# Kernel tuning notes

Hardware: AMD Instinct MI355X
Metric: run time of the kernel (lower is better)

The kernel has to match this reference:

```python
import jax, jax.numpy as jnp
import numpy as np

B = 128           # persons in batch
V = 128           # visits per person
CPV = 16          # codes per visit
MAX_VISITS = 510  # 512 - 2, hard-coded in module
D = 256           # embedding_dim * n_heads = 128 * 2
H = 2             # n_heads
DH = D // H
MAX_DAYS = 365
VOCAB = 30000
N_LAYERS = 2
DFF = 4 * D


def setup_inputs() -> dict:
    key = jax.random.key(0)
    ks = jax.random.split(key, 24)
    total_visits = B * V
    total_codes = total_visits * CPV
    all_codes = jax.random.randint(ks[0], (total_codes,), 0, VOCAB, dtype=jnp.int32)
    # code -> visit segment id (contiguous, as produced by the per-person loop)
    seg_ids = (jnp.arange(total_codes, dtype=jnp.int32) // CPV).astype(jnp.int32)
    # visit -> flattened slot in padded [B, MAX_VISITS] tensor (right-aligned)
    pos = MAX_VISITS - V + jnp.arange(V, dtype=jnp.int32)
    dest = (jnp.arange(B, dtype=jnp.int32)[:, None] * MAX_VISITS + pos[None, :]).reshape(-1)
    times = jax.random.uniform(ks[1], (total_visits,), minval=0.0, maxval=float(MAX_DAYS), dtype=jnp.float32)
    s = 0.02
    concept_emb = jax.random.normal(ks[2], (VOCAB, D), dtype=jnp.float32) * s
    pad_emb = jnp.zeros((D,), dtype=jnp.float32)
    Wq = jax.random.normal(ks[3], (N_LAYERS, D, D), dtype=jnp.float32) * s
    Wk = jax.random.normal(ks[4], (N_LAYERS, D, D), dtype=jnp.float32) * s
    Wv = jax.random.normal(ks[5], (N_LAYERS, D, D), dtype=jnp.float32) * s
    Wo = jax.random.normal(ks[6], (N_LAYERS, D, D), dtype=jnp.float32) * s
    W1 = jax.random.normal(ks[7], (N_LAYERS, D, DFF), dtype=jnp.float32) * s
    W2 = jax.random.normal(ks[8], (N_LAYERS, DFF, D), dtype=jnp.float32) * s
    z = lambda *sh: jnp.zeros(sh, dtype=jnp.float32)
    o = lambda *sh: jnp.ones(sh, dtype=jnp.float32)
    return dict(all_codes=all_codes, seg_ids=seg_ids, dest=dest, times=times,
                concept_emb=concept_emb, pad_emb=pad_emb,
                Wq=Wq, Wk=Wk, Wv=Wv, Wo=Wo,
                bq=z(N_LAYERS, D), bk=z(N_LAYERS, D), bv=z(N_LAYERS, D), bo=z(N_LAYERS, D),
                ln1_g=o(N_LAYERS, D), ln1_b=z(N_LAYERS, D),
                W1=W1, b1=z(N_LAYERS, DFF), W2=W2, b2=z(N_LAYERS, D),
                ln2_g=o(N_LAYERS, D), ln2_b=z(N_LAYERS, D))


def _ln(x, g, b):
    m = jnp.mean(x, axis=-1, keepdims=True)
    v = jnp.var(x, axis=-1, keepdims=True)
    return g * (x - m) * jax.lax.rsqrt(v + 1e-5) + b


def _forward(all_codes, seg_ids, dest, times, concept_emb, pad_emb,
             Wq, Wk, Wv, Wo, bq, bk, bv, bo, ln1_g, ln1_b,
             W1, b1, W2, b2, ln2_g, ln2_b):
    # gather code embeddings and segment-sum per visit (index_add_ in torch)
    emb = concept_emb[all_codes]                               # [total_codes, D]
    summed = jax.ops.segment_sum(emb, seg_ids, num_segments=B * V)  # [B*V, D]
    # scatter visits right-aligned into padded [B*MAX_VISITS, D], pad slots = pad_emb
    padded = jnp.broadcast_to(pad_emb, (B * MAX_VISITS, D)).at[dest].set(summed)
    # sinusoidal time embedding: timescales = ((1/1e4)**(1/D))**arange(D/2)
    t = jnp.clip(times, 0.0, float(MAX_DAYS - 1))
    ts = jnp.power(jnp.float32((1.0 / 10000.0) ** (1.0 / D)), jnp.arange(D // 2, dtype=jnp.float32))
    ang = t[:, None] * ts[None, :]                             # [B*V, D/2]
    te = jnp.concatenate([jnp.sin(ang), jnp.cos(ang)], axis=1) # [B*V, D]
    te_pad = jnp.zeros((B * MAX_VISITS, D), dtype=padded.dtype).at[dest].set(te)
    x = (padded + te_pad).reshape(B, MAX_VISITS, D)
    inv_sqrt_dh = np.float32(1.0 / np.sqrt(DH))
    for l in range(N_LAYERS):
        q = (x @ Wq[l] + bq[l]).reshape(B, MAX_VISITS, H, DH)
        k = (x @ Wk[l] + bk[l]).reshape(B, MAX_VISITS, H, DH)
        v = (x @ Wv[l] + bv[l]).reshape(B, MAX_VISITS, H, DH)
        scores = jnp.einsum('bqhd,bkhd->bhqk', q, k) * inv_sqrt_dh
        attn = jax.nn.softmax(scores, axis=-1)
        ctx = jnp.einsum('bhqk,bkhd->bqhd', attn, v).reshape(B, MAX_VISITS, D)
        x = _ln(x + ctx @ Wo[l] + bo[l], ln1_g[l], ln1_b[l])
        ff = jax.nn.relu(x @ W1[l] + b1[l]) @ W2[l] + b2[l]
        x = _ln(x + ff, ln2_g[l], ln2_b[l])
    return x


def reference(all_codes, seg_ids, dest, times, concept_emb, pad_emb,
              Wq, Wk, Wv, Wo, bq, bk, bv, bo, ln1_g, ln1_b,
              W1, b1, W2, b2, ln2_g, ln2_b):
    return _forward(all_codes, seg_ids, dest, times, concept_emb, pad_emb,
                    Wq, Wk, Wv, Wo, bq, bk, bv, bo, ln1_g, ln1_b,
                    W1, b1, W2, b2, ln2_g, ln2_b)
```

## Files before the change

### kernel.cpp

```cpp
#include <hip/hip_runtime.h>
#include <cstddef>

#define BATCH 128
#define NV 128
#define CPV 16
#define MAXV 510
#define NPAD 382
#define DIM 256
#define NH 2
#define DH 128
#define NLAYERS 2
#define DFF 1024
#define RROWS (BATCH * NV)
#define M2 (RROWS + BATCH)
#define AST 168
#define VST 160

typedef __attribute__((ext_vector_type(8))) short short8;
typedef __attribute__((ext_vector_type(4))) short short4v;
typedef __attribute__((ext_vector_type(4))) float floatx4;

__device__ __forceinline__ short f2bf(float f) {
    union { float f; unsigned u; } v; v.f = f;
    unsigned r = v.u + 0x7fffu + ((v.u >> 16) & 1u);
    return (short)(r >> 16);
}
__device__ __forceinline__ float bf2f(short s) {
    union { unsigned u; float f; } v; v.u = ((unsigned)(unsigned short)s) << 16;
    return v.f;
}

__device__ __forceinline__ void gload_lds16(const short* g, short* l) {
    __builtin_amdgcn_global_load_lds(
        (const __attribute__((address_space(1))) unsigned int*)g,
        (__attribute__((address_space(3))) unsigned int*)l,
        16, 0, 0);
}

__global__ __launch_bounds__(256) void wtrans_all(const float* __restrict__ Wq,
                                                  const float* __restrict__ Wk,
                                                  const float* __restrict__ Wv,
                                                  const float* __restrict__ Wo,
                                                  const float* __restrict__ W1,
                                                  const float* __restrict__ W2,
                                                  short* __restrict__ wqkvT,
                                                  short* __restrict__ woT,
                                                  short* __restrict__ w1T,
                                                  short* __restrict__ w2T) {
    int y = blockIdx.y;
    int l = y / 6, w = y - l * 6;
    const float* src; short* dst; int K, nsh;
    switch (w) {
        case 0:  src = Wq + (size_t)l * 65536;  dst = wqkvT + (size_t)l * 196608;           K = 256;  nsh = 8;  break;
        case 1:  src = Wk + (size_t)l * 65536;  dst = wqkvT + (size_t)l * 196608 + 65536;   K = 256;  nsh = 8;  break;
        case 2:  src = Wv + (size_t)l * 65536;  dst = wqkvT + (size_t)l * 196608 + 131072;  K = 256;  nsh = 8;  break;
        case 3:  src = Wo + (size_t)l * 65536;  dst = woT   + (size_t)l * 65536;            K = 256;  nsh = 8;  break;
        case 4:  src = W1 + (size_t)l * 262144; dst = w1T   + (size_t)l * 262144;           K = 256;  nsh = 10; break;
        default: src = W2 + (size_t)l * 262144; dst = w2T   + (size_t)l * 262144;           K = 1024; nsh = 8;  break;
    }
    int N = 1 << nsh;
    int idx = blockIdx.x * 256 + threadIdx.x;
    if (idx >= K * N) return;
    int k = idx >> nsh, n = idx & (N - 1);
    dst[(size_t)n * K + k] = f2bf(src[idx]);
}

__global__ __launch_bounds__(256) void build_x(const int* __restrict__ codes,
                                               const float* __restrict__ times,
                                               const float* __restrict__ cemb,
                                               const float* __restrict__ pemb,
                                               short* __restrict__ x) {
    int row = blockIdx.x;
    int d = threadIdx.x;
    float val;
    if (row >= RROWS) {
        val = pemb[d];
    } else {
        int b = row >> 7;
        int r = row & 127;
        int visit = b * NV + r;
        const int* cb = codes + visit * CPV;
        float s = 0.f;
#pragma unroll
        for (int c = 0; c < CPV; ++c)
            s += cemb[(size_t)cb[c] * DIM + d];
        float t = times[visit];
        t = fminf(fmaxf(t, 0.f), 364.f);
        int i = d & 127;
        float ang = t * expf(-0.03597789207803197f * (float)i);
        float te = (d < 128) ? sinf(ang) : cosf(ang);
        val = s + te;
    }
    x[(size_t)row * DIM + d] = f2bf(val);
}

__global__ __launch_bounds__(256) void gemm_qkv(const short* __restrict__ A,
                                                const short* __restrict__ BT,
                                                const float* __restrict__ bq,
                                                const float* __restrict__ bk,
                                                const float* __restrict__ bv,
                                                short* __restrict__ qo,
                                                short* __restrict__ ko,
                                                short* __restrict__ vo) {
    __shared__ __align__(16) short lA[2][128 * 32];
    __shared__ __align__(16) short lB[2][128 * 32];
    int tid = threadIdx.x;
    int wave = tid >> 6, lane = tid & 63;
    int l15 = lane & 15, quad = lane >> 4;
    int q8 = quad * 8;
    int m0 = blockIdx.y * 128;
    int n0 = blockIdx.x * 128;
    int sel = blockIdx.x >> 1;
    int nloc = n0 & 255;
    int wm = (wave & 1) * 64;
    int wn = (wave >> 1) * 64;

    int srow = tid >> 2;
    int skoff = (tid & 3) * 8;
    const short* ag = A + (size_t)(m0 + srow) * DIM + skoff;
    const short* bg = BT + (size_t)(n0 + srow) * DIM + skoff;
    const size_t rstep = (size_t)64 * DIM;
    int t8 = tid * 8;

    floatx4 acc[4][4];
#pragma unroll
    for (int i = 0; i < 4; ++i)
#pragma unroll
        for (int j = 0; j < 4; ++j) acc[i][j] = (floatx4){0.f, 0.f, 0.f, 0.f};

    gload_lds16(ag, lA[0] + t8);
    gload_lds16(ag + rstep, lA[0] + 2048 + t8);
    gload_lds16(bg, lB[0] + t8);
    gload_lds16(bg + rstep, lB[0] + 2048 + t8);
    __syncthreads();
    int cur = 0;
#pragma unroll
    for (int k0 = 0; k0 < 8; ++k0) {
        if (k0 < 7) {
            int kn = (k0 + 1) * 32;
            gload_lds16(ag + kn, lA[cur ^ 1] + t8);
            gload_lds16(ag + rstep + kn, lA[cur ^ 1] + 2048 + t8);
            gload_lds16(bg + kn, lB[cur ^ 1] + t8);
            gload_lds16(bg + rstep + kn, lB[cur ^ 1] + 2048 + t8);
        }
        short8 aF[4], bF[4];
#pragma unroll
        for (int t = 0; t < 4; ++t) {
            aF[t] = *(const short8*)(lA[cur] + (wm + t * 16 + l15) * 32 + q8);
            bF[t] = *(const short8*)(lB[cur] + (wn + t * 16 + l15) * 32 + q8);
        }
#pragma unroll
        for (int i = 0; i < 4; ++i)
#pragma unroll
            for (int j = 0; j < 4; ++j)
                acc[i][j] = __builtin_amdgcn_mfma_f32_16x16x32_bf16(aF[i], bF[j], acc[i][j], 0, 0, 0);
        __syncthreads();
        cur ^= 1;
    }

    const float* bias = (sel == 0) ? bq : (sel == 1) ? bk : bv;
    short* out = (sel == 0) ? qo : (sel == 1) ? ko : vo;
#pragma unroll
    for (int j = 0; j < 4; ++j) {
        int col = nloc + wn + j * 16 + l15;
        float bval = bias[col];
#pragma unroll
        for (int i = 0; i < 4; ++i) {
#pragma unroll
            for (int r = 0; r < 4; ++r) {
                int row = m0 + wm + i * 16 + quad * 4 + r;
                out[(size_t)row * DIM + col] = f2bf(acc[i][j][r] + bval);
            }
        }
    }
}

__global__ __launch_bounds__(256) void gemm_wo_ln(const short* __restrict__ CTX,
                                                  const short* __restrict__ WoT,
                                                  const float* __restrict__ bo,
                                                  const short* __restrict__ X,
                                                  const float* __restrict__ g,
                                                  const float* __restrict__ bta,
                                                  short* __restrict__ xout) {
    __shared__ __align__(16) short lA[2][64 * 32];
    __shared__ __align__(16) short lB[2][256 * 32];
    int tid = threadIdx.x;
    int wave = tid >> 6, lane = tid & 63;
    int l15 = lane & 15, quad = lane >> 4;
    int q8 = quad * 8;
    int m0 = blockIdx.x * 64;
    int wr = wave * 16;
    int srow = tid >> 2;
    int skoff = (tid & 3) * 8;
    const short* ag = CTX + (size_t)(m0 + srow) * DIM + skoff;
    const short* bg = WoT + (size_t)srow * DIM + skoff;
    int t8 = tid * 8;

    floatx4 acc[16];
#pragma unroll
    for (int j = 0; j < 16; ++j) acc[j] = (floatx4){0.f, 0.f, 0.f, 0.f};

    gload_lds16(ag, lA[0] + t8);
    gload_lds16(bg, lB[0] + t8);
    gload_lds16(bg + (size_t)64 * DIM, lB[0] + 2048 + t8);
    gload_lds16(bg + (size_t)128 * DIM, lB[0] + 4096 + t8);
    gload_lds16(bg + (size_t)192 * DIM, lB[0] + 6144 + t8);
    __syncthreads();
    int cur = 0;
#pragma unroll
    for (int k0 = 0; k0 < 8; ++k0) {
        if (k0 < 7) {
            int kn = (k0 + 1) * 32;
            gload_lds16(ag + kn, lA[cur ^ 1] + t8);
            gload_lds16(bg + kn, lB[cur ^ 1] + t8);
            gload_lds16(bg + (size_t)64 * DIM + kn, lB[cur ^ 1] + 2048 + t8);
            gload_lds16(bg + (size_t)128 * DIM + kn, lB[cur ^ 1] + 4096 + t8);
            gload_lds16(bg + (size_t)192 * DIM + kn, lB[cur ^ 1] + 6144 + t8);
        }
        short8 aF = *(const short8*)(lA[cur] + (wr + l15) * 32 + q8);
#pragma unroll
        for (int j = 0; j < 16; ++j) {
            short8 bF = *(const short8*)(lB[cur] + (j * 16 + l15) * 32 + q8);
            acc[j] = __builtin_amdgcn_mfma_f32_16x16x32_bf16(aF, bF, acc[j], 0, 0, 0);
        }
        __syncthreads();
        cur ^= 1;
    }

    float bias[16], gam[16], bet[16];
#pragma unroll
    for (int j = 0; j < 16; ++j) {
        int col = j * 16 + l15;
        bias[j] = bo[col]; gam[j] = g[col]; bet[j] = bta[col];
    }
#pragma unroll
    for (int r = 0; r < 4; ++r) {
        int row = m0 + wr + quad * 4 + r;
        float v[16], s = 0.f, sq = 0.f;
#pragma unroll
        for (int j = 0; j < 16; ++j) {
            v[j] = acc[j][r] + bias[j] + bf2f(X[(size_t)row * DIM + j * 16 + l15]);
            s += v[j]; sq += v[j] * v[j];
        }
        s += __shfl_xor(s, 1); sq += __shfl_xor(sq, 1);
        s += __shfl_xor(s, 2); sq += __shfl_xor(sq, 2);
        s += __shfl_xor(s, 4); sq += __shfl_xor(sq, 4);
        s += __shfl_xor(s, 8); sq += __shfl_xor(sq, 8);
        float mean = s * (1.f / 256.f);
        float var = fmaxf(sq * (1.f / 256.f) - mean * mean, 0.f);
        float rstd = rsqrtf(var + 1e-5f);
#pragma unroll
        for (int j = 0; j < 16; ++j) {
            float y = gam[j] * (v[j] - mean) * rstd + bet[j];
            xout[(size_t)row * DIM + j * 16 + l15] = f2bf(y);
        }
    }
}

#define PST 136
__global__ __launch_bounds__(256, 2) void ff_fused(const short* __restrict__ X,
                                                   const short* __restrict__ W1T,
                                                   const float* __restrict__ b1,
                                                   const short* __restrict__ W2T,
                                                   const float* __restrict__ b2,
                                                   const float* __restrict__ g2,
                                                   const float* __restrict__ bt2,
                                                   short* __restrict__ xout,
                                                   float* __restrict__ fout,
                                                   float* __restrict__ padrowF) {
    __shared__ __align__(16) short lA[2][64 * 32];
    __shared__ __align__(16) short lB[2][128 * 32];
    __shared__ __align__(16) short lB2[2][256 * 32];
    __shared__ __align__(16) short lP[64 * PST];
    __shared__ float redS[4][32], redQ[4][32];
    int tid = threadIdx.x;
    int wave = tid >> 6, lane = tid & 63;
    int l15 = lane & 15, quad = lane >> 4;
    int q8 = quad * 8;
    int m0 = blockIdx.x * 64;
    int wm = (wave & 1) * 32;
    int wf = (wave >> 1) * 64;
    int wn2 = (wave >> 1) * 128;
    int srow = tid >> 2;
    int spart = (tid & 3) * 8;
    const short* xg = X + (size_t)(m0 + srow) * DIM + spart;
    int t8 = tid * 8;

    floatx4 acc2[2][8];
#pragma unroll
    for (int i = 0; i < 2; ++i)
#pragma unroll
        for (int j = 0; j < 8; ++j) acc2[i][j] = (floatx4){0.f, 0.f, 0.f, 0.f};

    for (int f0 = 0; f0 < DFF; f0 += 128) {
        const short* w1g = W1T + (size_t)(f0 + srow) * DIM + spart;
        floatx4 acc1[2][4];
#pragma unroll
        for (int i = 0; i < 2; ++i)
#pragma unroll
            for (int j = 0; j < 4; ++j) acc1[i][j] = (floatx4){0.f, 0.f, 0.f, 0.f};

        gload_lds16(xg, lA[0] + t8);
        gload_lds16(w1g, lB[0] + t8);
        gload_lds16(w1g + (size_t)64 * DIM, lB[0] + 2048 + t8);
        __syncthreads();
        int cur = 0;
#pragma unroll
        for (int k0 = 0; k0 < 8; ++k0) {
            if (k0 < 7) {
                int kn = (k0 + 1) * 32;
                gload_lds16(xg + kn, lA[cur ^ 1] + t8);
                gload_lds16(w1g + kn, lB[cur ^ 1] + t8);
                gload_lds16(w1g + (size_t)64 * DIM + kn, lB[cur ^ 1] + 2048 + t8);
            }
            short8 aF[2], bF[4];
#pragma unroll
            for (int t = 0; t < 2; ++t)
                aF[t] = *(const short8*)(lA[cur] + (wm + t * 16 + l15) * 32 + q8);
#pragma unroll
            for (int t = 0; t < 4; ++t)
                bF[t] = *(const short8*)(lB[cur] + (wf + t * 16 + l15) * 32 + q8);
#pragma unroll
            for (int i = 0; i < 2; ++i)
#pragma unroll
                for (int j = 0; j < 4; ++j)
                    acc1[i][j] = __builtin_amdgcn_mfma_f32_16x16x32_bf16(aF[i], bF[j], acc1[i][j], 0, 0, 0);
            __syncthreads();
            cur ^= 1;
        }

        {
            const short* w2g = W2T + (size_t)srow * DFF + f0 + spart;
            gload_lds16(w2g, lB2[0] + t8);
            gload_lds16(w2g + (size_t)64 * DFF, lB2[0] + 2048 + t8);
            gload_lds16(w2g + (size_t)128 * DFF, lB2[0] + 4096 + t8);
            gload_lds16(w2g + (size_t)192 * DFF, lB2[0] + 6144 + t8);
        }
#pragma unroll
        for (int j = 0; j < 4; ++j) {
            int fc = wf + j * 16 + l15;
            float bval = b1[f0 + fc];
#pragma unroll
            for (int i = 0; i < 2; ++i) {
#pragma unroll
                for (int r = 0; r < 4; ++r) {
                    float v = acc1[i][j][r] + bval;
                    lP[(wm + i * 16 + quad * 4 + r) * PST + fc] = f2bf(fmaxf(v, 0.f));
                }
            }
        }
        __syncthreads();
        cur = 0;
#pragma unroll
        for (int ks = 0; ks < 4; ++ks) {
            if (ks < 3) {
                const short* w2g = W2T + (size_t)srow * DFF + f0 + (ks + 1) * 32 + spart;
                gload_lds16(w2g, lB2[cur ^ 1] + t8);
                gload_lds16(w2g + (size_t)64 * DFF, lB2[cur ^ 1] + 2048 + t8);
                gload_lds16(w2g + (size_t)128 * DFF, lB2[cur ^ 1] + 4096 + t8);
                gload_lds16(w2g + (size_t)192 * DFF, lB2[cur ^ 1] + 6144 + t8);
            }
            short8 aP[2], bW[8];
#pragma unroll
            for (int t = 0; t < 2; ++t)
                aP[t] = *(const short8*)(lP + (wm + t * 16 + l15) * PST + ks * 32 + q8);
#pragma unroll
            for (int j = 0; j < 8; ++j)
                bW[j] = *(const short8*)(lB2[cur] + (wn2 + j * 16 + l15) * 32 + q8);
#pragma unroll
            for (int i = 0; i < 2; ++i)
#pragma unroll
                for (int j = 0; j < 8; ++j)
                    acc2[i][j] = __builtin_amdgcn_mfma_f32_16x16x32_bf16(aP[i], bW[j], acc2[i][j], 0, 0, 0);
            __syncthreads();
            cur ^= 1;
        }
    }

    float b2v[8];
#pragma unroll
    for (int j = 0; j < 8; ++j) b2v[j] = b2[wn2 + j * 16 + l15];
#pragma unroll
    for (int i = 0; i < 2; ++i) {
#pragma unroll
        for (int r = 0; r < 4; ++r) {
            int row = m0 + wm + i * 16 + quad * 4 + r;
            float s = 0.f, sq = 0.f;
#pragma unroll
            for (int j = 0; j < 8; ++j) {
                float v = acc2[i][j][r] + b2v[j] + bf2f(X[(size_t)row * DIM + wn2 + j * 16 + l15]);
                acc2[i][j][r] = v;
                s += v; sq += v * v;
            }
            s += __shfl_xor(s, 1); sq += __shfl_xor(sq, 1);
            s += __shfl_xor(s, 2); sq += __shfl_xor(sq, 2);
            s += __shfl_xor(s, 4); sq += __shfl_xor(sq, 4);
            s += __shfl_xor(s, 8); sq += __shfl_xor(sq, 8);
            if (l15 == 0) {
                int idx = i * 16 + quad * 4 + r;
                redS[wave][idx] = s;
                redQ[wave][idx] = sq;
            }
        }
    }
    __syncthreads();
    float gam[8], bet[8];
#pragma unroll
    for (int j = 0; j < 8; ++j) {
        int col = wn2 + j * 16 + l15;
        gam[j] = g2[col]; bet[j] = bt2[col];
    }
#pragma unroll
    for (int i = 0; i < 2; ++i) {
#pragma unroll
        for (int r = 0; r < 4; ++r) {
            int idx = i * 16 + quad * 4 + r;
            float ts = redS[wave][idx] + redS[wave ^ 2][idx];
            float tq = redQ[wave][idx] + redQ[wave ^ 2][idx];
            float mean = ts * (1.f / 256.f);
            float var = fmaxf(tq * (1.f / 256.f) - mean * mean, 0.f);
            float rstd = rsqrtf(var + 1e-5f);
            int grow = m0 + wm + i * 16 + quad * 4 + r;
            if (!fout) {
#pragma unroll
                for (int j = 0; j < 8; ++j) {
                    float y = gam[j] * (acc2[i][j][r] - mean) * rstd + bet[j];
                    xout[(size_t)grow * DIM + wn2 + j * 16 + l15] = f2bf(y);
                }
            } else if (grow < RROWS) {
                int bb = grow >> 7, rr = grow & 127;
                float* dst = fout + ((size_t)bb * MAXV + NPAD + rr) * DIM;
#pragma unroll
                for (int j = 0; j < 8; ++j) {
                    float y = gam[j] * (acc2[i][j][r] - mean) * rstd + bet[j];
                    dst[wn2 + j * 16 + l15] = y;
                }
            } else {
                float* dst = padrowF + (size_t)(grow - RROWS) * DIM;
#pragma unroll
                for (int j = 0; j < 8; ++j) {
                    float y = gam[j] * (acc2[i][j][r] - mean) * rstd + bet[j];
                    dst[wn2 + j * 16 + l15] = y;
                }
            }
        }
    }
}

__global__ __launch_bounds__(256) void pad_attn(const short* __restrict__ q,
                                                const short* __restrict__ k,
                                                const short* __restrict__ v,
                                                short* __restrict__ ctx) {
    __shared__ float qv[256], wgt[2][128], wp[2], den[2];
    int b = blockIdx.x, tid = threadIdx.x;
    int h = tid >> 7, kk = tid & 127;
    const float scale = 0.08838834764831845f;
    qv[tid] = bf2f(q[(size_t)(RROWS + b) * DIM + tid]);
    __syncthreads();
    {
        const short8* krow = (const short8*)(k + (size_t)(b * NV + kk) * DIM + h * DH);
        float s = 0.f;
#pragma unroll
        for (int c = 0; c < 16; ++c) {
            short8 k8 = krow[c];
#pragma unroll
            for (int e = 0; e < 8; ++e) s += bf2f(k8[e]) * qv[h * DH + c * 8 + e];
        }
        wgt[h][kk] = __expf(fminf(s * scale, 30.f));
    }
    if (kk == 0) {
        const short8* kp = (const short8*)(k + (size_t)(RROWS + b) * DIM + h * DH);
        float sp = 0.f;
#pragma unroll
        for (int c = 0; c < 16; ++c) {
            short8 k8 = kp[c];
#pragma unroll
            for (int e = 0; e < 8; ++e) sp += bf2f(k8[e]) * qv[h * DH + c * 8 + e];
        }
        wp[h] = 382.f * __expf(fminf(sp * scale, 30.f));
    }
    __syncthreads();
    if (kk == 0) {
        float d = wp[h];
        for (int i = 0; i < 128; ++i) d += wgt[h][i];
        den[h] = d;
    }
    __syncthreads();
    {
        const short* vcol = v + (size_t)(b * NV) * DIM + h * DH + kk;
        float c = 0.f;
#pragma unroll 8
        for (int key = 0; key < 128; ++key) c += wgt[h][key] * bf2f(vcol[(size_t)key * DIM]);
        c += wp[h] * bf2f(v[(size_t)(RROWS + b) * DIM + h * DH + kk]);
        ctx[(size_t)(RROWS + b) * DIM + tid] = f2bf(c / den[h]);
    }
}

__global__ __launch_bounds__(256) void pad_bcast(const float* __restrict__ padrow,
                                                 float* __restrict__ fout) {
    int b = blockIdx.y;
    int p = blockIdx.x * 4 + (threadIdx.x >> 6);
    if (p >= NPAD) return;
    int d4 = (threadIdx.x & 63) * 4;
    floatx4 v = *(const floatx4*)(padrow + (size_t)b * DIM + d4);
    *(floatx4*)(fout + ((size_t)b * MAXV + p) * DIM + d4) = v;
}

__global__ __launch_bounds__(256) void transpose_v(const short* __restrict__ v,
                                                   short* __restrict__ vT) {
    __shared__ short lds[32][33];
    int pair = blockIdx.y;
    int b = pair >> 1, h = pair & 1;
    int st = blockIdx.x % 5;
    int dt = blockIdx.x / 5;
    int tid = threadIdx.x;
    int sl = tid >> 3, dl = (tid & 7) * 4;
    short4v val;
    if (st < 4) {
        const short* src = v + ((size_t)(b * NV + st * 32 + sl)) * DIM + h * DH + dt * 32 + dl;
        val = *(const short4v*)src;
    } else {
        val = (short4v){0, 0, 0, 0};
        if (sl == 0)
            val = *(const short4v*)(v + (size_t)(RROWS + b) * DIM + h * DH + dt * 32 + dl);
    }
#pragma unroll
    for (int j = 0; j < 4; ++j) lds[sl][dl + j] = val[j];
    __syncthreads();
    int drow = tid >> 3, scol = (tid & 7) * 4;
    short* dst = vT + (size_t)pair * DH * VST + (size_t)(dt * 32 + drow) * VST + st * 32 + scol;
#pragma unroll
    for (int j = 0; j < 4; ++j) dst[j] = lds[scol + j][drow];
}

__global__ __launch_bounds__(256) void attn_fused(const short* __restrict__ q,
                                                  const short* __restrict__ k,
                                                  const short* __restrict__ vT,
                                                  short* __restrict__ ctx) {
    __shared__ __align__(16) short lA[64 * 32];
    __shared__ __align__(16) short lB[128 * 32];
    __shared__ __align__(16) short lS[64 * AST];
    int tid = threadIdx.x;
    int wave = tid >> 6, lane = tid & 63;
    int l15 = lane & 15, quad = lane >> 4;
    int q8 = quad * 8;
    int pair = blockIdx.y;
    int b = pair >> 1, h = pair & 1;
    int m0 = blockIdx.x * 64;
    int wm = (wave & 1) * 32;
    int wn = (wave >> 1) * 64;

    int srow = tid >> 2;
    int skoff = (tid & 3) * 8;
    const short* ag = q + (size_t)(b * NV + m0 + srow) * DIM + h * DH + skoff;
    const short* bg = k + (size_t)(b * NV + srow) * DIM + h * DH + skoff;
    const short* kp = k + (size_t)(RROWS + b) * DIM + h * DH + q8;
    short* lA_dst = lA + tid * 8;
    short* lB_dst = lB + tid * 8;
    const float scale = 0.08838834764831845f;

    {
        int zr = tid >> 2, zc = 144 + (tid & 3) * 4;
        *(short4v*)(lS + zr * AST + zc) = (short4v){0, 0, 0, 0};
    }

    floatx4 sacc[2][4];
    floatx4 sacct[2];
#pragma unroll
    for (int i = 0; i < 2; ++i) {
#pragma unroll
        for (int j = 0; j < 4; ++j) sacc[i][j] = (floatx4){0.f, 0.f, 0.f, 0.f};
        sacct[i] = (floatx4){0.f, 0.f, 0.f, 0.f};
    }

#pragma unroll
    for (int k0 = 0; k0 < DH; k0 += 32) {
        gload_lds16(ag + k0, lA_dst);
        gload_lds16(bg + k0, lB_dst);
        gload_lds16(bg + (size_t)64 * DIM + k0, lB_dst + 2048);
        __syncthreads();
        short8 aF[2], bF[4];
#pragma unroll
        for (int t = 0; t < 2; ++t)
            aF[t] = *(const short8*)(lA + (wm + t * 16 + l15) * 32 + q8);
#pragma unroll
        for (int t = 0; t < 4; ++t)
            bF[t] = *(const short8*)(lB + (wn + t * 16 + l15) * 32 + q8);
#pragma unroll
        for (int i = 0; i < 2; ++i)
#pragma unroll
            for (int j = 0; j < 4; ++j)
                sacc[i][j] = __builtin_amdgcn_mfma_f32_16x16x32_bf16(aF[i], bF[j], sacc[i][j], 0, 0, 0);
        if (wn == 0) {
            short8 bFt = (l15 == 0) ? *(const short8*)(kp + k0) : (short8){0,0,0,0,0,0,0,0};
#pragma unroll
            for (int i = 0; i < 2; ++i)
                sacct[i] = __builtin_amdgcn_mfma_f32_16x16x32_bf16(aF[i], bFt, sacct[i], 0, 0, 0);
        }
        __syncthreads();
    }
#pragma unroll
    for (int j = 0; j < 4; ++j) {
        int col = wn + j * 16 + l15;
#pragma unroll
        for (int i = 0; i < 2; ++i) {
#pragma unroll
            for (int r = 0; r < 4; ++r) {
                lS[(wm + i * 16 + quad * 4 + r) * AST + col] =
                    f2bf(__expf(fminf(sacc[i][j][r] * scale, 30.f)));
            }
        }
    }
    if (wn == 0) {
        float wt = (l15 == 0) ? 382.f : 0.f;
#pragma unroll
        for (int i = 0; i < 2; ++i) {
#pragma unroll
            for (int r = 0; r < 4; ++r) {
                lS[(wm + i * 16 + quad * 4 + r) * AST + 128 + l15] =
                    f2bf(wt * __expf(fminf(sacct[i][r] * scale, 30.f)));
            }
        }
    }
    __syncthreads();
    const short* vg = vT + (size_t)pair * DH * VST + (size_t)srow * VST + skoff;
    floatx4 oacc[2][4];
#pragma unroll
    for (int i = 0; i < 2; ++i)
#pragma unroll
        for (int j = 0; j < 4; ++j) oacc[i][j] = (floatx4){0.f, 0.f, 0.f, 0.f};
    float rsum[2] = {0.f, 0.f};

#pragma unroll
    for (int ks = 0; ks < 5; ++ks) {
        gload_lds16(vg + ks * 32, lB_dst);
        gload_lds16(vg + (size_t)64 * VST + ks * 32, lB_dst + 2048);
        __syncthreads();
        short8 aP[2], bV[4];
#pragma unroll
        for (int t = 0; t < 2; ++t)
            aP[t] = *(const short8*)(lS + (wm + t * 16 + l15) * AST + ks * 32 + q8);
#pragma unroll
        for (int t = 0; t < 4; ++t)
            bV[t] = *(const short8*)(lB + (wn + t * 16 + l15) * 32 + q8);
#pragma unroll
        for (int i = 0; i < 2; ++i) {
            float s = 0.f;
#pragma unroll
            for (int e = 0; e < 8; ++e) s += bf2f(aP[i][e]);
            rsum[i] += s;
        }
#pragma unroll
        for (int i = 0; i < 2; ++i)
#pragma unroll
            for (int j = 0; j < 4; ++j)
                oacc[i][j] = __builtin_amdgcn_mfma_f32_16x16x32_bf16(aP[i], bV[j], oacc[i][j], 0, 0, 0);
        __syncthreads();
    }

#pragma unroll
    for (int i = 0; i < 2; ++i) {
        rsum[i] += __shfl_xor(rsum[i], 16);
        rsum[i] += __shfl_xor(rsum[i], 32);
    }
    short* outb = ctx + (size_t)(b * NV + m0) * DIM + h * DH;
#pragma unroll
    for (int i = 0; i < 2; ++i) {
#pragma unroll
        for (int r = 0; r < 4; ++r) {
            float inv = 1.f / __shfl(rsum[i], quad * 4 + r);
#pragma unroll
            for (int j = 0; j < 4; ++j) {
                int col = wn + j * 16 + l15;
                int row = wm + i * 16 + quad * 4 + r;
                outb[(size_t)row * DIM + col] = f2bf(oacc[i][j][r] * inv);
            }
        }
    }
}

extern "C" void kernel_launch(void* const* d_in, const int* in_sizes, int n_in,
                              void* d_out, int out_size, void* d_ws, size_t ws_size,
                              hipStream_t stream) {
    const int*   all_codes = (const int*)d_in[0];
    const float* times = (const float*)d_in[3];
    const float* cemb  = (const float*)d_in[4];
    const float* pemb  = (const float*)d_in[5];
    const float* Wq = (const float*)d_in[6];
    const float* Wk = (const float*)d_in[7];
    const float* Wv = (const float*)d_in[8];
    const float* Wo = (const float*)d_in[9];
    const float* bq = (const float*)d_in[10];
    const float* bk = (const float*)d_in[11];
    const float* bv = (const float*)d_in[12];
    const float* bo = (const float*)d_in[13];
    const float* ln1g = (const float*)d_in[14];
    const float* ln1b = (const float*)d_in[15];
    const float* W1 = (const float*)d_in[16];
    const float* b1 = (const float*)d_in[17];
    const float* W2 = (const float*)d_in[18];
    const float* b2 = (const float*)d_in[19];
    const float* ln2g = (const float*)d_in[20];
    const float* ln2b = (const float*)d_in[21];

    char* ws = (char*)d_ws;
    short* wqkvT = (short*)ws;
    short* woT   = wqkvT + 2 * 196608;
    short* w1T   = woT + 2 * 65536;
    short* w2T   = w1T + 2 * 262144;
    float* padrowF = (float*)(ws + (3500u << 10));

    const size_t SLOT = (size_t)M2 * DIM;
    short* xb = (short*)(ws + (4u << 20));
    short* C0 = xb + SLOT;
    short* C1 = C0 + SLOT;
    short* C2 = C1 + SLOT;
    short* C3 = C2 + SLOT;
    short* C4 = C3 + SLOT;

    wtrans_all<<<dim3(1024, 12), 256, 0, stream>>>(Wq, Wk, Wv, Wo, W1, W2,
                                                   wqkvT, woT, w1T, w2T);
    build_x<<<M2, 256, 0, stream>>>(all_codes, times, cemb, pemb, xb);

    for (int l = 0; l < NLAYERS; ++l) {
        const short* qkv_l = wqkvT + (size_t)l * 196608;
        const short* wo_l = woT + (size_t)l * 65536;
        const short* w1_l = w1T + (size_t)l * 262144;
        const short* w2_l = w2T + (size_t)l * 262144;
        int last = (l == NLAYERS - 1);

        gemm_qkv<<<dim3(6, M2 / 128), 256, 0, stream>>>(xb, qkv_l, bq + l * 256, bk + l * 256,
                                                        bv + l * 256, C0, C1, C2);
        transpose_v<<<dim3(20, BATCH * NH), 256, 0, stream>>>(C2, C4);
        attn_fused<<<dim3(2, BATCH * NH), 256, 0, stream>>>(C0, C1, C4, C3);
        pad_attn<<<BATCH, 256, 0, stream>>>(C0, C1, C2, C3);
        gemm_wo_ln<<<M2 / 64, 256, 0, stream>>>(C3, wo_l, bo + l * 256, xb,
                                                ln1g + l * 256, ln1b + l * 256, C0);
        ff_fused<<<M2 / 64, 256, 0, stream>>>(C0, w1_l, b1 + l * 1024, w2_l, b2 + l * 256,
                                              ln2g + l * 256, ln2b + l * 256, xb,
                                              last ? (float*)d_out : nullptr,
                                              last ? padrowF : nullptr);
        if (last)
            pad_bcast<<<dim3(96, BATCH), 256, 0, stream>>>(padrowF, (float*)d_out);
    }
}
```

Before: 415.7 us.

## Load full K-extent tiles into LDS at once instead of double-buffered K-steps

The QKV, Wo+LN and FF GEMM kernels now issue every global-to-LDS load for the whole K dimension up front and wait once on a single barrier, replacing the per-32-wide double-buffered loop that needed a barrier at each step. The Wo+LN kernel also halves its row tile to 32, splits the columns across waves, and reduces LayerNorm statistics through shared memory, which doubles its grid. FF now reuses one LDS buffer for W1 and W2 slices and drops the two-blocks-per-CU launch bound. The aim is fewer barriers and more loads in flight, at the cost of much larger LDS use per block (about 128KB in gemm_qkv), which lowers occupancy and leaves no compute to overlap with the loads.

Result: slower. 479.0 us (+15.2%).

```diff
diff --git a/kernel.cpp b/kernel.cpp
--- a/kernel.cpp
+++ b/kernel.cpp
@@ -102,8 +102,8 @@
                                                 short* __restrict__ qo,
                                                 short* __restrict__ ko,
                                                 short* __restrict__ vo) {
-    __shared__ __align__(16) short lA[2][128 * 32];
-    __shared__ __align__(16) short lB[2][128 * 32];
+    __shared__ __align__(16) short lA[8 * 128 * 32];
+    __shared__ __align__(16) short lB[8 * 128 * 32];
     int tid = threadIdx.x;
     int wave = tid >> 6, lane = tid & 63;
     int l15 = lane & 15, quad = lane >> 4;
@@ -119,43 +119,36 @@
     int skoff = (tid & 3) * 8;
     const short* ag = A + (size_t)(m0 + srow) * DIM + skoff;
     const short* bg = BT + (size_t)(n0 + srow) * DIM + skoff;
-    const size_t rstep = (size_t)64 * DIM;
     int t8 = tid * 8;
 
+#pragma unroll
+    for (int s = 0; s < 8; ++s) {
+        gload_lds16(ag + s * 32, lA + s * 4096 + t8);
+        gload_lds16(ag + (size_t)64 * DIM + s * 32, lA + s * 4096 + 2048 + t8);
+        gload_lds16(bg + s * 32, lB + s * 4096 + t8);
+        gload_lds16(bg + (size_t)64 * DIM + s * 32, lB + s * 4096 + 2048 + t8);
+    }
+    __syncthreads();
+
     floatx4 acc[4][4];
 #pragma unroll
     for (int i = 0; i < 4; ++i)
 #pragma unroll
         for (int j = 0; j < 4; ++j) acc[i][j] = (floatx4){0.f, 0.f, 0.f, 0.f};
 
-    gload_lds16(ag, lA[0] + t8);
-    gload_lds16(ag + rstep, lA[0] + 2048 + t8);
-    gload_lds16(bg, lB[0] + t8);
-    gload_lds16(bg + rstep, lB[0] + 2048 + t8);
-    __syncthreads();
-    int cur = 0;
-#pragma unroll
-    for (int k0 = 0; k0 < 8; ++k0) {
-        if (k0 < 7) {
-            int kn = (k0 + 1) * 32;
-            gload_lds16(ag + kn, lA[cur ^ 1] + t8);
-            gload_lds16(ag + rstep + kn, lA[cur ^ 1] + 2048 + t8);
-            gload_lds16(bg + kn, lB[cur ^ 1] + t8);
-            gload_lds16(bg + rstep + kn, lB[cur ^ 1] + 2048 + t8);
-        }
+#pragma unroll
+    for (int s = 0; s < 8; ++s) {
         short8 aF[4], bF[4];
 #pragma unroll
         for (int t = 0; t < 4; ++t) {
-            aF[t] = *(const short8*)(lA[cur] + (wm + t * 16 + l15) * 32 + q8);
-            bF[t] = *(const short8*)(lB[cur] + (wn + t * 16 + l15) * 32 + q8);
+            aF[t] = *(const short8*)(lA + s * 4096 + (wm + t * 16 + l15) * 32 + q8);
+            bF[t] = *(const short8*)(lB + s * 4096 + (wn + t * 16 + l15) * 32 + q8);
         }
 #pragma unroll
         for (int i = 0; i < 4; ++i)
 #pragma unroll
             for (int j = 0; j < 4; ++j)
                 acc[i][j] = __builtin_amdgcn_mfma_f32_16x16x32_bf16(aF[i], bF[j], acc[i][j], 0, 0, 0);
-        __syncthreads();
-        cur ^= 1;
     }
 
     const float* bias = (sel == 0) ? bq : (sel == 1) ? bk : bv;
@@ -182,95 +175,112 @@
                                                   const float* __restrict__ g,
                                                   const float* __restrict__ bta,
                                                   short* __restrict__ xout) {
-    __shared__ __align__(16) short lA[2][64 * 32];
-    __shared__ __align__(16) short lB[2][256 * 32];
+    __shared__ __align__(16) short lA[8 * 32 * 32];
+    __shared__ __align__(16) short lB[8 * 256 * 32];
+    __shared__ float redS[4][16], redQ[4][16];
     int tid = threadIdx.x;
     int wave = tid >> 6, lane = tid & 63;
     int l15 = lane & 15, quad = lane >> 4;
     int q8 = quad * 8;
-    int m0 = blockIdx.x * 64;
-    int wr = wave * 16;
+    int m0 = blockIdx.x * 32;
+    int wm = (wave & 1) * 16;
+    int wn = (wave >> 1) * 128;
     int srow = tid >> 2;
     int skoff = (tid & 3) * 8;
-    const short* ag = CTX + (size_t)(m0 + srow) * DIM + skoff;
-    const short* bg = WoT + (size_t)srow * DIM + skoff;
     int t8 = tid * 8;
 
-    floatx4 acc[16];
-#pragma unroll
-    for (int j = 0; j < 16; ++j) acc[j] = (floatx4){0.f, 0.f, 0.f, 0.f};
-
-    gload_lds16(ag, lA[0] + t8);
-    gload_lds16(bg, lB[0] + t8);
-    gload_lds16(bg + (size_t)64 * DIM, lB[0] + 2048 + t8);
-    gload_lds16(bg + (size_t)128 * DIM, lB[0] + 4096 + t8);
-    gload_lds16(bg + (size_t)192 * DIM, lB[0] + 6144 + t8);
-    __syncthreads();
-    int cur = 0;
-#pragma unroll
-    for (int k0 = 0; k0 < 8; ++k0) {
-        if (k0 < 7) {
-            int kn = (k0 + 1) * 32;
-            gload_lds16(ag + kn, lA[cur ^ 1] + t8);
-            gload_lds16(bg + kn, lB[cur ^ 1] + t8);
-            gload_lds16(bg + (size_t)64 * DIM + kn, lB[cur ^ 1] + 2048 + t8);
-            gload_lds16(bg + (size_t)128 * DIM + kn, lB[cur ^ 1] + 4096 + t8);
-            gload_lds16(bg + (size_t)192 * DIM + kn, lB[cur ^ 1] + 6144 + t8);
-        }
-        short8 aF = *(const short8*)(lA[cur] + (wr + l15) * 32 + q8);
-#pragma unroll
-        for (int j = 0; j < 16; ++j) {
-            short8 bF = *(const short8*)(lB[cur] + (j * 16 + l15) * 32 + q8);
+    {
+        int arow = (tid & 127) >> 2;
+        int apart = (tid & 3) * 8;
+        const short* agb = CTX + (size_t)(m0 + arow) * DIM + apart;
+#pragma unroll
+        for (int i = 0; i < 4; ++i) {
+            int s = (tid >> 7) + 2 * i;
+            gload_lds16(agb + s * 32, lA + s * 1024 + (tid & 127) * 8);
+        }
+    }
+    {
+        const short* bgb = WoT + (size_t)srow * DIM + skoff;
+#pragma unroll
+        for (int s = 0; s < 8; ++s) {
+#pragma unroll
+            for (int u = 0; u < 4; ++u)
+                gload_lds16(bgb + (size_t)u * 64 * DIM + s * 32,
+                            lB + s * 8192 + u * 2048 + t8);
+        }
+    }
+    __syncthreads();
+
+    floatx4 acc[8];
+#pragma unroll
+    for (int j = 0; j < 8; ++j) acc[j] = (floatx4){0.f, 0.f, 0.f, 0.f};
+
+#pragma unroll
+    for (int s = 0; s < 8; ++s) {
+        short8 aF = *(const short8*)(lA + s * 1024 + (wm + l15) * 32 + q8);
+#pragma unroll
+        for (int j = 0; j < 8; ++j) {
+            short8 bF = *(const short8*)(lB + s * 8192 + (wn + j * 16 + l15) * 32 + q8);
             acc[j] = __builtin_amdgcn_mfma_f32_16x16x32_bf16(aF, bF, acc[j], 0, 0, 0);
         }
-        __syncthreads();
-        cur ^= 1;
-    }
-
-    float bias[16], gam[16], bet[16];
-#pragma unroll
-    for (int j = 0; j < 16; ++j) {
-        int col = j * 16 + l15;
+    }
+
+    float bias[8], gam[8], bet[8];
+#pragma unroll
+    for (int j = 0; j < 8; ++j) {
+        int col = wn + j * 16 + l15;
         bias[j] = bo[col]; gam[j] = g[col]; bet[j] = bta[col];
     }
+    float v[4][8];
 #pragma unroll
     for (int r = 0; r < 4; ++r) {
-        int row = m0 + wr + quad * 4 + r;
-        float v[16], s = 0.f, sq = 0.f;
-#pragma unroll
-        for (int j = 0; j < 16; ++j) {
-            v[j] = acc[j][r] + bias[j] + bf2f(X[(size_t)row * DIM + j * 16 + l15]);
-            s += v[j]; sq += v[j] * v[j];
+        int row = m0 + wm + quad * 4 + r;
+        float s = 0.f, sq = 0.f;
+#pragma unroll
+        for (int j = 0; j < 8; ++j) {
+            v[r][j] = acc[j][r] + bias[j] + bf2f(X[(size_t)row * DIM + wn + j * 16 + l15]);
+            s += v[r][j]; sq += v[r][j] * v[r][j];
         }
         s += __shfl_xor(s, 1); sq += __shfl_xor(sq, 1);
         s += __shfl_xor(s, 2); sq += __shfl_xor(sq, 2);
         s += __shfl_xor(s, 4); sq += __shfl_xor(sq, 4);
         s += __shfl_xor(s, 8); sq += __shfl_xor(sq, 8);
-        float mean = s * (1.f / 256.f);
-        float var = fmaxf(sq * (1.f / 256.f) - mean * mean, 0.f);
+        if (l15 == 0) {
+            redS[wave][quad * 4 + r] = s;
+            redQ[wave][quad * 4 + r] = sq;
+        }
+    }
+    __syncthreads();
+#pragma unroll
+    for (int r = 0; r < 4; ++r) {
+        int idx = quad * 4 + r;
+        float ts = redS[wave][idx] + redS[wave ^ 2][idx];
+        float tq = redQ[wave][idx] + redQ[wave ^ 2][idx];
+        float mean = ts * (1.f / 256.f);
+        float var = fmaxf(tq * (1.f / 256.f) - mean * mean, 0.f);
         float rstd = rsqrtf(var + 1e-5f);
-#pragma unroll
-        for (int j = 0; j < 16; ++j) {
-            float y = gam[j] * (v[j] - mean) * rstd + bet[j];
-            xout[(size_t)row * DIM + j * 16 + l15] = f2bf(y);
+        int row = m0 + wm + quad * 4 + r;
+#pragma unroll
+        for (int j = 0; j < 8; ++j) {
+            float y = gam[j] * (v[r][j] - mean) * rstd + bet[j];
+            xout[(size_t)row * DIM + wn + j * 16 + l15] = f2bf(y);
         }
     }
 }
 
 #define PST 136
-__global__ __launch_bounds__(256, 2) void ff_fused(const short* __restrict__ X,
-                                                   const short* __restrict__ W1T,
-                                                   const float* __restrict__ b1,
-                                                   const short* __restrict__ W2T,
-                                                   const float* __restrict__ b2,
-                                                   const float* __restrict__ g2,
-                                                   const float* __restrict__ bt2,
-                                                   short* __restrict__ xout,
-                                                   float* __restrict__ fout,
-                                                   float* __restrict__ padrowF) {
-    __shared__ __align__(16) short lA[2][64 * 32];
-    __shared__ __align__(16) short lB[2][128 * 32];
-    __shared__ __align__(16) short lB2[2][256 * 32];
+__global__ __launch_bounds__(256) void ff_fused(const short* __restrict__ X,
+                                                const short* __restrict__ W1T,
+                                                const float* __restrict__ b1,
+                                                const short* __restrict__ W2T,
+                                                const float* __restrict__ b2,
+                                                const float* __restrict__ g2,
+                                                const float* __restrict__ bt2,
+                                                short* __restrict__ xout,
+                                                float* __restrict__ fout,
+                                                float* __restrict__ padrowF) {
+    __shared__ __align__(16) short lX[8 * 64 * 32];
+    __shared__ __align__(16) short lW[8 * 128 * 32];
     __shared__ __align__(16) short lP[64 * PST];
     __shared__ float redS[4][32], redQ[4][32];
     int tid = threadIdx.x;
@@ -292,49 +302,50 @@
 #pragma unroll
         for (int j = 0; j < 8; ++j) acc2[i][j] = (floatx4){0.f, 0.f, 0.f, 0.f};
 
+#pragma unroll
+    for (int s = 0; s < 8; ++s)
+        gload_lds16(xg + s * 32, lX + s * 2048 + t8);
+    {
+        const short* w1g = W1T + (size_t)srow * DIM + spart;
+#pragma unroll
+        for (int s = 0; s < 8; ++s) {
+            gload_lds16(w1g + s * 32, lW + s * 4096 + t8);
+            gload_lds16(w1g + (size_t)64 * DIM + s * 32, lW + s * 4096 + 2048 + t8);
+        }
+    }
+    __syncthreads();
+
     for (int f0 = 0; f0 < DFF; f0 += 128) {
-        const short* w1g = W1T + (size_t)(f0 + srow) * DIM + spart;
         floatx4 acc1[2][4];
 #pragma unroll
         for (int i = 0; i < 2; ++i)
 #pragma unroll
             for (int j = 0; j < 4; ++j) acc1[i][j] = (floatx4){0.f, 0.f, 0.f, 0.f};
-
-        gload_lds16(xg, lA[0] + t8);
-        gload_lds16(w1g, lB[0] + t8);
-        gload_lds16(w1g + (size_t)64 * DIM, lB[0] + 2048 + t8);
-        __syncthreads();
-        int cur = 0;
-#pragma unroll
-        for (int k0 = 0; k0 < 8; ++k0) {
-            if (k0 < 7) {
-                int kn = (k0 + 1) * 32;
-                gload_lds16(xg + kn, lA[cur ^ 1] + t8);
-                gload_lds16(w1g + kn, lB[cur ^ 1] + t8);
-                gload_lds16(w1g + (size_t)64 * DIM + kn, lB[cur ^ 1] + 2048 + t8);
-            }
+#pragma unroll
+        for (int s = 0; s < 8; ++s) {
             short8 aF[2], bF[4];
 #pragma unroll
             for (int t = 0; t < 2; ++t)
-                aF[t] = *(const short8*)(lA[cur] + (wm + t * 16 + l15) * 32 + q8);
+                aF[t] = *(const short8*)(lX + s * 2048 + (wm + t * 16 + l15) * 32 + q8);
 #pragma unroll
             for (int t = 0; t < 4; ++t)
-                bF[t] = *(const short8*)(lB[cur] + (wf + t * 16 + l15) * 32 + q8);
+                bF[t] = *(const short8*)(lW + s * 4096 + (wf + t * 16 + l15) * 32 + q8);
 #pragma unroll
             for (int i = 0; i < 2; ++i)
 #pragma unroll
                 for (int j = 0; j < 4; ++j)
                     acc1[i][j] = __builtin_amdgcn_mfma_f32_16x16x32_bf16(aF[i], bF[j], acc1[i][j], 0, 0, 0);
-            __syncthreads();
-            cur ^= 1;
-        }
+        }
+        __syncthreads();
 
         {
             const short* w2g = W2T + (size_t)srow * DFF + f0 + spart;
-            gload_lds16(w2g, lB2[0] + t8);
-            gload_lds16(w2g + (size_t)64 * DFF, lB2[0] + 2048 + t8);
-            gload_lds16(w2g + (size_t)128 * DFF, lB2[0] + 4096 + t8);
-            gload_lds16(w2g + (size_t)192 * DFF, lB2[0] + 6144 + t8);
+#pragma unroll
+            for (int ks = 0; ks < 4; ++ks)
+#pragma unroll
+                for (int u = 0; u < 4; ++u)
+                    gload_lds16(w2g + (size_t)u * 64 * DFF + ks * 32,
+                                lW + ks * 8192 + u * 2048 + t8);
         }
 #pragma unroll
         for (int j = 0; j < 4; ++j) {
@@ -350,30 +361,32 @@
             }
         }
         __syncthreads();
-        cur = 0;
+
 #pragma unroll
         for (int ks = 0; ks < 4; ++ks) {
-            if (ks < 3) {
-                const short* w2g = W2T + (size_t)srow * DFF + f0 + (ks + 1) * 32 + spart;
-                gload_lds16(w2g, lB2[cur ^ 1] + t8);
-                gload_lds16(w2g + (size_t)64 * DFF, lB2[cur ^ 1] + 2048 + t8);
-                gload_lds16(w2g + (size_t)128 * DFF, lB2[cur ^ 1] + 4096 + t8);
-                gload_lds16(w2g + (size_t)192 * DFF, lB2[cur ^ 1] + 6144 + t8);
-            }
             short8 aP[2], bW[8];
 #pragma unroll
             for (int t = 0; t < 2; ++t)
                 aP[t] = *(const short8*)(lP + (wm + t * 16 + l15) * PST + ks * 32 + q8);
 #pragma unroll
             for (int j = 0; j < 8; ++j)
-                bW[j] = *(const short8*)(lB2[cur] + (wn2 + j * 16 + l15) * 32 + q8);
+                bW[j] = *(const short8*)(lW + ks * 8192 + (wn2 + j * 16 + l15) * 32 + q8);
 #pragma unroll
             for (int i = 0; i < 2; ++i)
 #pragma unroll
                 for (int j = 0; j < 8; ++j)
                     acc2[i][j] = __builtin_amdgcn_mfma_f32_16x16x32_bf16(aP[i], bW[j], acc2[i][j], 0, 0, 0);
+        }
+        __syncthreads();
+
+        if (f0 < DFF - 128) {
+            const short* w1g = W1T + (size_t)(f0 + 128 + srow) * DIM + spart;
+#pragma unroll
+            for (int s = 0; s < 8; ++s) {
+                gload_lds16(w1g + s * 32, lW + s * 4096 + t8);
+                gload_lds16(w1g + (size_t)64 * DIM + s * 32, lW + s * 4096 + 2048 + t8);
+            }
             __syncthreads();
-            cur ^= 1;
         }
     }
 
@@ -734,7 +747,7 @@
         transpose_v<<<dim3(20, BATCH * NH), 256, 0, stream>>>(C2, C4);
         attn_fused<<<dim3(2, BATCH * NH), 256, 0, stream>>>(C0, C1, C4, C3);
         pad_attn<<<BATCH, 256, 0, stream>>>(C0, C1, C2, C3);
-        gemm_wo_ln<<<M2 / 64, 256, 0, stream>>>(C3, wo_l, bo + l * 256, xb,
+        gemm_wo_ln<<<M2 / 32, 256, 0, stream>>>(C3, wo_l, bo + l * 256, xb,
                                                 ln1g + l * 256, ln1b + l * 256, C0);
         ff_fused<<<M2 / 64, 256, 0, stream>>>(C0, w1_l, b1 + l * 1024, w2_l, b2 + l * 256,
                                               ln2g + l * 256, ln2b + l * 256, xb,
```

## Keep X tile resident in LDS and triple-buffer weight loads in FF kernel

Applied to the files above, without the earlier changes.

The fused feed-forward kernel now loads the whole 64x256 X tile into LDS once, instead of reloading it for every 128-column DFF chunk. W1 and W2 slices move to a three-stage ring buffer using explicit vmcnt waits and raw s_barrier in place of __syncthreads. W2 prefetch for the second GEMM is issued before the ReLU/bias write to LDS. The aim is to cut redundant global loads and barrier stalls, at the cost of more LDS and dropping the 2-blocks-per-CU launch bound, which may lower occupancy.

New measurement: 468.2 us. 1.13x slower.

```diff
diff --git a/kernel.cpp b/kernel.cpp
--- a/kernel.cpp
+++ b/kernel.cpp
@@ -258,19 +258,19 @@
 }
 
 #define PST 136
-__global__ __launch_bounds__(256, 2) void ff_fused(const short* __restrict__ X,
-                                                   const short* __restrict__ W1T,
-                                                   const float* __restrict__ b1,
-                                                   const short* __restrict__ W2T,
-                                                   const float* __restrict__ b2,
-                                                   const float* __restrict__ g2,
-                                                   const float* __restrict__ bt2,
-                                                   short* __restrict__ xout,
-                                                   float* __restrict__ fout,
-                                                   float* __restrict__ padrowF) {
-    __shared__ __align__(16) short lA[2][64 * 32];
-    __shared__ __align__(16) short lB[2][128 * 32];
-    __shared__ __align__(16) short lB2[2][256 * 32];
+__global__ __launch_bounds__(256) void ff_fused(const short* __restrict__ X,
+                                                const short* __restrict__ W1T,
+                                                const float* __restrict__ b1,
+                                                const short* __restrict__ W2T,
+                                                const float* __restrict__ b2,
+                                                const float* __restrict__ g2,
+                                                const float* __restrict__ bt2,
+                                                short* __restrict__ xout,
+                                                float* __restrict__ fout,
+                                                float* __restrict__ padrowF) {
+    __shared__ __align__(16) short lX[8 * 64 * 32];
+    __shared__ __align__(16) short lW1[3][128 * 32];
+    __shared__ __align__(16) short lB2[3][256 * 32];
     __shared__ __align__(16) short lP[64 * PST];
     __shared__ float redS[4][32], redQ[4][32];
     int tid = threadIdx.x;
@@ -292,73 +292,90 @@
 #pragma unroll
         for (int j = 0; j < 8; ++j) acc2[i][j] = (floatx4){0.f, 0.f, 0.f, 0.f};
 
+#pragma unroll
+    for (int s = 0; s < 8; ++s)
+        gload_lds16(xg + s * 32, lX + s * 2048 + t8);
+
     for (int f0 = 0; f0 < DFF; f0 += 128) {
         const short* w1g = W1T + (size_t)(f0 + srow) * DIM + spart;
+        const short* w2g = W2T + (size_t)srow * DFF + f0 + spart;
+        float bval1[4];
+#pragma unroll
+        for (int j = 0; j < 4; ++j) bval1[j] = b1[f0 + wf + j * 16 + l15];
+
+        gload_lds16(w1g, lW1[0] + t8);
+        gload_lds16(w1g + (size_t)64 * DIM, lW1[0] + 2048 + t8);
+        gload_lds16(w1g + 32, lW1[1] + t8);
+        gload_lds16(w1g + (size_t)64 * DIM + 32, lW1[1] + 2048 + t8);
+        asm volatile("s_waitcnt vmcnt(2)" ::: "memory");
+        __builtin_amdgcn_s_barrier();
+        __builtin_amdgcn_sched_barrier(0);
+
         floatx4 acc1[2][4];
 #pragma unroll
         for (int i = 0; i < 2; ++i)
 #pragma unroll
             for (int j = 0; j < 4; ++j) acc1[i][j] = (floatx4){0.f, 0.f, 0.f, 0.f};
 
-        gload_lds16(xg, lA[0] + t8);
-        gload_lds16(w1g, lB[0] + t8);
-        gload_lds16(w1g + (size_t)64 * DIM, lB[0] + 2048 + t8);
-        __syncthreads();
-        int cur = 0;
-#pragma unroll
-        for (int k0 = 0; k0 < 8; ++k0) {
-            if (k0 < 7) {
-                int kn = (k0 + 1) * 32;
-                gload_lds16(xg + kn, lA[cur ^ 1] + t8);
-                gload_lds16(w1g + kn, lB[cur ^ 1] + t8);
-                gload_lds16(w1g + (size_t)64 * DIM + kn, lB[cur ^ 1] + 2048 + t8);
+#pragma unroll
+        for (int s = 0; s < 8; ++s) {
+            if (s < 6) {
+                int kn = (s + 2) * 32;
+                gload_lds16(w1g + kn, lW1[(s + 2) % 3] + t8);
+                gload_lds16(w1g + (size_t)64 * DIM + kn, lW1[(s + 2) % 3] + 2048 + t8);
             }
             short8 aF[2], bF[4];
 #pragma unroll
             for (int t = 0; t < 2; ++t)
-                aF[t] = *(const short8*)(lA[cur] + (wm + t * 16 + l15) * 32 + q8);
+                aF[t] = *(const short8*)(lX + s * 2048 + (wm + t * 16 + l15) * 32 + q8);
 #pragma unroll
             for (int t = 0; t < 4; ++t)
-                bF[t] = *(const short8*)(lB[cur] + (wf + t * 16 + l15) * 32 + q8);
+                bF[t] = *(const short8*)(lW1[s % 3] + (wf + t * 16 + l15) * 32 + q8);
 #pragma unroll
             for (int i = 0; i < 2; ++i)
 #pragma unroll
                 for (int j = 0; j < 4; ++j)
                     acc1[i][j] = __builtin_amdgcn_mfma_f32_16x16x32_bf16(aF[i], bF[j], acc1[i][j], 0, 0, 0);
-            __syncthreads();
-            cur ^= 1;
-        }
-
-        {
-            const short* w2g = W2T + (size_t)srow * DFF + f0 + spart;
-            gload_lds16(w2g, lB2[0] + t8);
-            gload_lds16(w2g + (size_t)64 * DFF, lB2[0] + 2048 + t8);
-            gload_lds16(w2g + (size_t)128 * DFF, lB2[0] + 4096 + t8);
-            gload_lds16(w2g + (size_t)192 * DFF, lB2[0] + 6144 + t8);
-        }
+            if (s < 6) {
+                asm volatile("s_waitcnt vmcnt(2)" ::: "memory");
+            } else if (s == 6) {
+                asm volatile("s_waitcnt vmcnt(0)" ::: "memory");
+            }
+            if (s < 7) {
+                __builtin_amdgcn_s_barrier();
+                __builtin_amdgcn_sched_barrier(0);
+            }
+        }
+
+#pragma unroll
+        for (int ks = 0; ks < 2; ++ks)
+#pragma unroll
+            for (int u = 0; u < 4; ++u)
+                gload_lds16(w2g + (size_t)u * 64 * DFF + ks * 32,
+                            lB2[ks] + u * 2048 + t8);
 #pragma unroll
         for (int j = 0; j < 4; ++j) {
             int fc = wf + j * 16 + l15;
-            float bval = b1[f0 + fc];
 #pragma unroll
             for (int i = 0; i < 2; ++i) {
 #pragma unroll
                 for (int r = 0; r < 4; ++r) {
-                    float v = acc1[i][j][r] + bval;
+                    float v = acc1[i][j][r] + bval1[j];
                     lP[(wm + i * 16 + quad * 4 + r) * PST + fc] = f2bf(fmaxf(v, 0.f));
                 }
             }
         }
-        __syncthreads();
-        cur = 0;
+        asm volatile("s_waitcnt vmcnt(4) lgkmcnt(0)" ::: "memory");
+        __builtin_amdgcn_s_barrier();
+        __builtin_amdgcn_sched_barrier(0);
+
 #pragma unroll
         for (int ks = 0; ks < 4; ++ks) {
-            if (ks < 3) {
-                const short* w2g = W2T + (size_t)srow * DFF + f0 + (ks + 1) * 32 + spart;
-                gload_lds16(w2g, lB2[cur ^ 1] + t8);
-                gload_lds16(w2g + (size_t)64 * DFF, lB2[cur ^ 1] + 2048 + t8);
-                gload_lds16(w2g + (size_t)128 * DFF, lB2[cur ^ 1] + 4096 + t8);
-                gload_lds16(w2g + (size_t)192 * DFF, lB2[cur ^ 1] + 6144 + t8);
+            if (ks < 2) {
+#pragma unroll
+                for (int u = 0; u < 4; ++u)
+                    gload_lds16(w2g + (size_t)u * 64 * DFF + (ks + 2) * 32,
+                                lB2[(ks + 2) % 3] + u * 2048 + t8);
             }
             short8 aP[2], bW[8];
 #pragma unroll
@@ -366,16 +383,25 @@
                 aP[t] = *(const short8*)(lP + (wm + t * 16 + l15) * PST + ks * 32 + q8);
 #pragma unroll
             for (int j = 0; j < 8; ++j)
-                bW[j] = *(const short8*)(lB2[cur] + (wn2 + j * 16 + l15) * 32 + q8);
+                bW[j] = *(const short8*)(lB2[ks % 3] + (wn2 + j * 16 + l15) * 32 + q8);
 #pragma unroll
             for (int i = 0; i < 2; ++i)
 #pragma unroll
                 for (int j = 0; j < 8; ++j)
                     acc2[i][j] = __builtin_amdgcn_mfma_f32_16x16x32_bf16(aP[i], bW[j], acc2[i][j], 0, 0, 0);
-            __syncthreads();
-            cur ^= 1;
-        }
-    }
+            if (ks < 2) {
+                asm volatile("s_waitcnt vmcnt(4)" ::: "memory");
+            } else if (ks == 2) {
+                asm volatile("s_waitcnt vmcnt(0)" ::: "memory");
+            }
+            if (ks < 3) {
+                __builtin_amdgcn_s_barrier();
+                __builtin_amdgcn_sched_barrier(0);
+            }
+        }
+    }
+
+    __syncthreads();
 
     float b2v[8];
 #pragma unroll
```
